# Kernel tuning notes

Hardware: AMD Instinct MI355X
Metric: run time of the kernel (lower is better)

## Reference

```python
import jax, jax.numpy as jnp
import numpy as np

MIN_SIZE = 16.0 / 800.0
PRE_NMS_TOP_K = 6000   # mode='test'
POST_NMS_TOP_K = 300   # mode='test'
IOU_THR = 0.7
H = W = 100
A = 9
N = H * W * A


def setup_inputs() -> dict:
    key = jax.random.key(0)
    k1, k2, k3 = jax.random.split(key, 3)
    pred_cls = jax.random.normal(k1, (1, H, W, 2 * A), dtype=jnp.float32)
    pred_reg = jax.random.normal(k2, (1, N, 4), dtype=jnp.float32) * 0.2
    # anchors as valid normalized xyxy boxes
    u = jax.random.uniform(k3, (N, 4), dtype=jnp.float32)
    cx = 0.05 + 0.9 * u[:, 0]
    cy = 0.05 + 0.9 * u[:, 1]
    w = 0.02 + 0.18 * u[:, 2]
    h = 0.02 + 0.18 * u[:, 3]
    anchor = jnp.stack([cx - w / 2, cy - h / 2, cx + w / 2, cy + h / 2], axis=1)
    return {"pred_cls": pred_cls, "pred_reg": pred_reg, "anchor": anchor}


def greedy_nms_mask(boxes, valid):
    # boxes: [K,4] sorted by descending score; valid: [K] bool
    K = boxes.shape[0]
    area = (boxes[:, 2] - boxes[:, 0]) * (boxes[:, 3] - boxes[:, 1])
    lt = jnp.maximum(boxes[:, None, :2], boxes[None, :, :2])   # [K,K,2]
    rb = jnp.minimum(boxes[:, None, 2:], boxes[None, :, 2:])
    wh = jnp.clip(rb - lt, 0.0)
    inter = wh[..., 0] * wh[..., 1]
    union = area[:, None] + area[None, :] - inter
    iou = inter / jnp.maximum(union, jnp.float32(1e-12))       # [K,K]
    idx = jnp.arange(K)

    def body(i, suppressed):
        keep_i = jnp.logical_not(suppressed[i]) & valid[i]
        return suppressed | (keep_i & (iou[i] > IOU_THR) & (idx > i))

    suppressed = jax.lax.fori_loop(0, K, body, jnp.zeros((K,), dtype=bool))
    return jnp.logical_not(suppressed) & valid


def reference(pred_cls, pred_reg, anchor):
    reg = pred_reg.reshape(-1, 4)                 # squeeze -> [N,4]
    # xy_to_cxcy(anchor)
    a_cxcy = jnp.concatenate([(anchor[:, 2:] + anchor[:, :2]) / 2,
                              anchor[:, 2:] - anchor[:, :2]], axis=1)
    # decode(reg, anchor_cxcy)
    cxcy = reg[:, :2] * a_cxcy[:, 2:] + a_cxcy[:, :2]
    wh = jnp.exp(reg[:, 2:]) * a_cxcy[:, 2:]
    # cxcy_to_xy(...).clamp(0,1)
    roi = jnp.clip(jnp.concatenate([cxcy - wh / 2, cxcy + wh / 2], axis=1), 0.0, 1.0)

    # objectness softmax over the 2-class logits
    probs = jax.nn.softmax(pred_cls.reshape(1, H, W, A, 2), axis=-1)[..., 1].reshape(-1)  # [N]

    # size filter
    ws = roi[:, 2] - roi[:, 0]
    hs = roi[:, 3] - roi[:, 1]
    size_ok = (hs >= MIN_SIZE) & (ws >= MIN_SIZE)
    masked_scores = jnp.where(size_ok, probs, -jnp.inf)

    # sort descending + take pre-NMS top-k (filtered boxes sort last)
    top_scores, top_idx = jax.lax.top_k(masked_scores, PRE_NMS_TOP_K)
    boxes = roi[top_idx]                           # [K,4]
    valid = size_ok[top_idx]

    kept = greedy_nms_mask(boxes, valid)           # [K] bool

    # first POST_NMS_TOP_K kept boxes in score order; pad with zeros
    rank = jnp.cumsum(kept.astype(jnp.int32)) - 1
    slot = jnp.where(kept & (rank < POST_NMS_TOP_K), rank, POST_NMS_TOP_K)
    out = jnp.zeros((POST_NMS_TOP_K, 4), dtype=boxes.dtype).at[slot].set(boxes, mode='drop')
    return out
```

## Files before the change

### kernel.cpp

```cpp
#include <hip/hip_runtime.h>
#include <stdint.h>

#pragma clang fp contract(off)

#define N_ANCH 90000
#define M_TOP  1024
#define M_L    512
#define NW_L   8
#define K_POST 300
#define CAP    2048
#define WINB   0x3D00
#define WINSZ  768
#define MIN_SIZE (16.0f / 800.0f)
#define IOU_THR  0.7f

#define NB_D 88
#define NB_C 32
#define GPB  704

#define SIDX(j) ((j) + ((j) >> 6))
#define SB_SZ   (M_L + NW_L)

#define OFF_CNT   0
#define OFF_HIST  64
#define OFF_MASK  64
#define OFF_CAND  135232
#define OFF_ROI   151616
#define OFF_KEYS  1591616
#define OFF_SBOX  1591616

__global__ void __launch_bounds__(1024)
decode_kernel(const float2* __restrict__ cls,
              const float4* __restrict__ reg,
              const float4* __restrict__ anc,
              float4* __restrict__ roi,
              unsigned* __restrict__ keys,
              unsigned short* __restrict__ hist,
              int* __restrict__ cnt) {
    __shared__ int lh[WINSZ];
    const int tid = threadIdx.x;
    const int bid = blockIdx.x;
    if (tid < WINSZ) lh[tid] = 0;
    if (bid == 0 && tid == 0) cnt[0] = 0;
    __syncthreads();

    const int n = bid * 1024 + tid;
    if (n < N_ANCH) {
        float4 a = anc[n];
        float4 r = reg[n];
        float aw  = a.z - a.x;
        float ah  = a.w - a.y;
        float acx = (a.z + a.x) * 0.5f;
        float acy = (a.w + a.y) * 0.5f;
        float cx = r.x * aw + acx;
        float cy = r.y * ah + acy;
        float w  = expf(r.z) * aw;
        float h  = expf(r.w) * ah;
        float x1 = fminf(fmaxf(cx - w * 0.5f, 0.0f), 1.0f);
        float y1 = fminf(fmaxf(cy - h * 0.5f, 0.0f), 1.0f);
        float x2 = fminf(fmaxf(cx + w * 0.5f, 0.0f), 1.0f);
        float y2 = fminf(fmaxf(cy + h * 0.5f, 0.0f), 1.0f);
        roi[n] = make_float4(x1, y1, x2, y2);

        float2 c = cls[n];
        float m  = fmaxf(c.x, c.y);
        float e0 = expf(c.x - m);
        float e1 = expf(c.y - m);
        float p  = e1 / (e0 + e1);

        bool ok = ((x2 - x1) >= MIN_SIZE) && ((y2 - y1) >= MIN_SIZE);
        unsigned key = ok ? (__float_as_uint(p) ^ 0x80000000u) : 0u;
        keys[n] = key;
        if (key != 0u) {
            int hb = (int)(key >> 16) - 0x8000;
            if (hb >= WINB) atomicAdd(&lh[hb - WINB], 1);
        }
    }
    __syncthreads();
    if (tid < WINSZ) hist[tid * NB_D + bid] = (unsigned short)lh[tid];
}

__global__ void __launch_bounds__(1024)
compact_kernel(const unsigned* __restrict__ keys,
               const unsigned short* __restrict__ hist,
               int* __restrict__ cnt,
               unsigned long long* __restrict__ cand) {
    __shared__ int rscan[1024];
    __shared__ unsigned s_thr;
    __shared__ int wcnt[16], wbase[16];
    __shared__ int s_base;
    const int t = threadIdx.x;

    int wsum = 0;
    if (t < WINSZ) {
        const int bin = WINSZ - 1 - t;
        const uint4* hp = (const uint4*)(hist + bin * NB_D);
#pragma unroll
        for (int q = 0; q < 11; ++q) {
            uint4 v = hp[q];
            wsum += (int)((v.x & 0xffffu) + (v.x >> 16) + (v.y & 0xffffu) + (v.y >> 16)
                        + (v.z & 0xffffu) + (v.z >> 16) + (v.w & 0xffffu) + (v.w >> 16));
        }
    }
    rscan[t] = wsum;
    __syncthreads();
    for (int off = 1; off < 1024; off <<= 1) {
        int add = (t >= off) ? rscan[t - off] : 0;
        __syncthreads();
        rscan[t] += add;
        __syncthreads();
    }
    if (t < WINSZ && rscan[t] >= M_TOP && (t == 0 || rscan[t - 1] < M_TOP))
        s_thr = ((unsigned)(0x8000 + WINB + (WINSZ - 1 - t))) << 16;
    if (t == 0 && rscan[WINSZ - 1] < M_TOP)
        s_thr = 0x80000000u;
    __syncthreads();
    const unsigned thr = s_thr;

    const uint4* k4 = (const uint4*)keys;
    const int g = blockIdx.x * GPB + t;
    const int gend0 = (blockIdx.x + 1) * GPB;
    const int gend = (gend0 < N_ANCH / 4) ? gend0 : (N_ANCH / 4);
    unsigned pm = 0;
    uint4 kv = make_uint4(0u, 0u, 0u, 0u);
    if (t < GPB && g < gend) {
        kv = k4[g];
        pm = (kv.x >= thr ? 1u : 0u) | (kv.y >= thr ? 2u : 0u)
           | (kv.z >= thr ? 4u : 0u) | (kv.w >= thr ? 8u : 0u);
    }
    unsigned long long b0 = __ballot((pm & 1u) != 0u);
    unsigned long long b1 = __ballot((pm & 2u) != 0u);
    unsigned long long b2 = __ballot((pm & 4u) != 0u);
    unsigned long long b3 = __ballot((pm & 8u) != 0u);
    const int ln = t & 63, wv = t >> 6;
    if (ln == 0)
        wcnt[wv] = __popcll(b0) + __popcll(b1) + __popcll(b2) + __popcll(b3);
    __syncthreads();
    if (t == 0) {
        int s = 0;
#pragma unroll
        for (int q = 0; q < 16; ++q) { wbase[q] = s; s += wcnt[q]; }
        s_base = s ? atomicAdd(cnt, s) : 0;
    }
    __syncthreads();
    if (pm) {
        unsigned long long lt = (ln == 0) ? 0ull : ((1ull << ln) - 1ull);
        int pos = s_base + wbase[wv]
                + __popcll(b0 & lt) + __popcll(b1 & lt) + __popcll(b2 & lt) + __popcll(b3 & lt);
        int n0 = g * 4;
        if (pm & 1u) { if (pos < CAP) cand[pos] = ((unsigned long long)kv.x << 32) | (unsigned)(~(unsigned)n0);       ++pos; }
        if (pm & 2u) { if (pos < CAP) cand[pos] = ((unsigned long long)kv.y << 32) | (unsigned)(~(unsigned)(n0 + 1)); ++pos; }
        if (pm & 4u) { if (pos < CAP) cand[pos] = ((unsigned long long)kv.z << 32) | (unsigned)(~(unsigned)(n0 + 2)); ++pos; }
        if (pm & 8u) { if (pos < CAP) cand[pos] = ((unsigned long long)kv.w << 32) | (unsigned)(~(unsigned)(n0 + 3)); ++pos; }
    }
}

__global__ void __launch_bounds__(1024)
rank_select_kernel(const unsigned long long* __restrict__ cand,
                   const int* __restrict__ cnt,
                   const float4* __restrict__ roi,
                   float4* __restrict__ sbox) {
    __shared__ unsigned long long s[CAP];
    __shared__ int red[1024];
    int tid = threadIdx.x;
    int c = cnt[0];
    if (c > CAP) c = CAP;
    for (int k = tid; k < CAP; k += 1024) s[k] = (k < c) ? cand[k] : 0ULL;
    __syncthreads();
    int e = tid & 63;
    int slice = tid >> 6;
    int i = blockIdx.x * 64 + e;
    unsigned long long v = (i < c) ? s[i] : 0ULL;
    int cnt_gt = 0;
    if (i < c) {
        int kbeg = slice * (CAP / 16);
        int kend = kbeg + (CAP / 16);
        if (kend > c) kend = c;
#pragma unroll 4
        for (int k = kbeg; k < kend; ++k)
            cnt_gt += (s[k] > v) ? 1 : 0;
    }
    red[tid] = cnt_gt;
    __syncthreads();
    if (slice == 0 && i < c) {
        int rank = 0;
#pragma unroll
        for (int q = 0; q < 16; ++q) rank += red[e + 64 * q];
        if (rank < M_TOP) {
            unsigned idx = ~((unsigned)v);
            sbox[rank] = roi[idx];
        }
    }
}

__global__ void __launch_bounds__(256)
mask_kernel(const float4* __restrict__ sbox,
            unsigned long long* __restrict__ mask) {
    __shared__ float4 sb[SB_SZ];
    int tid = threadIdx.x;
#pragma unroll
    for (int q = 0; q < M_L / 256; ++q) {
        int j = tid + q * 256;
        sb[SIDX(j)] = sbox[j];
    }
    __syncthreads();
    int wid = blockIdx.x * 256 + tid;
    int i = wid >> 3;
    int w = wid & 7;
    unsigned long long bits = 0;
    int j0 = w << 6;
    if (j0 + 63 > i) {
        float4 bi = sb[SIDX(i)];
        float ai = (bi.z - bi.x) * (bi.w - bi.y);
        for (int b = 0; b < 64; ++b) {
            int j = j0 + b;
            if (j > i) {
                float4 bj = sb[SIDX(j)];
                float xx1 = fmaxf(bi.x, bj.x);
                float yy1 = fmaxf(bi.y, bj.y);
                float xx2 = fminf(bi.z, bj.z);
                float yy2 = fminf(bi.w, bj.w);
                float ww = fmaxf(xx2 - xx1, 0.0f);
                float hh = fmaxf(yy2 - yy1, 0.0f);
                float inter = ww * hh;
                float aj = (bj.z - bj.x) * (bj.w - bj.y);
                float uni = ai + aj - inter;
                float iou = inter / fmaxf(uni, 1e-12f);
                if (iou > IOU_THR) bits |= 1ull << b;
            }
        }
    }
    mask[wid] = bits;
}

__device__ __forceinline__ unsigned long long readlane64(unsigned long long v, int sl) {
    unsigned lo = (unsigned)__builtin_amdgcn_readlane((int)(unsigned)v, sl);
    unsigned hi = (unsigned)__builtin_amdgcn_readlane((int)(unsigned)(v >> 32), sl);
    return ((unsigned long long)hi << 32) | lo;
}

__global__ void __launch_bounds__(256)
walk_kernel(const unsigned long long* __restrict__ mask,
            const float4* __restrict__ sbox,
            const int* __restrict__ cnt,
            float4* __restrict__ out) {
    __shared__ unsigned long long lmask[M_L * NW_L];
    __shared__ int s_keep[K_POST];
    __shared__ int s_kc;
    const int tid = threadIdx.x;

    {
        const uint4* src = (const uint4*)mask;
        uint4* dst = (uint4*)lmask;
#pragma unroll
        for (int q = 0; q < (M_L * NW_L) / 2 / 256; ++q)
            dst[tid + q * 256] = src[tid + q * 256];
    }
    __syncthreads();

    if (tid < 64) {
        int lane = tid;
        int c_eff = cnt[0];
        if (c_eff > M_TOP) c_eff = M_TOP;

        unsigned long long diag[NW_L];
#pragma unroll
        for (int cc = 0; cc < NW_L; ++cc)
            diag[cc] = lmask[(((cc << 6) | lane) << 3) + cc];

        unsigned long long remw = 0;
        int w = lane & 7;
        int kgrp = lane >> 3;
        int kc = 0;
        bool stop = false;
#pragma unroll
        for (int cc = 0; cc < NW_L; ++cc) {
            int base = cc << 6;
            unsigned long long valid =
                (c_eff >= base + 64) ? ~0ull
              : ((c_eff <= base) ? 0ull : ((1ull << (c_eff - base)) - 1ull));
            unsigned long long live = valid & ~readlane64(remw, cc);
            unsigned long long keptbits = 0;
            while (live) {
                int b = __ffsll((unsigned long long)live) - 1;
                keptbits |= 1ull << b;
                if (lane == 0) s_keep[kc] = base + b;
                ++kc;
                if (kc >= K_POST) { stop = true; break; }
                live &= ~readlane64(diag[cc], b);
                live &= ~(1ull << b);
            }
            if (stop) break;
            if (cc == NW_L - 1) break;
            if (keptbits) {
                int nk = __popcll(keptbits);
                int mypos = 0;
                if (lane < nk) {
                    unsigned long long tmp = keptbits;
                    for (int p = 0; p < lane; ++p) tmp &= tmp - 1;
                    mypos = base + (__ffsll((unsigned long long)tmp) - 1);
                }
                unsigned long long acc = 0;
#pragma unroll
                for (int r = 0; r < 8; ++r) {
                    int kg = (r << 3) | kgrp;
                    int row = __shfl(mypos, kg);
                    unsigned long long v = (kg < nk) ? lmask[(row << 3) + w] : 0ull;
                    acc |= v;
                }
                acc |= __shfl_xor(acc, 8);
                acc |= __shfl_xor(acc, 16);
                acc |= __shfl_xor(acc, 32);
                remw |= acc;
            }
        }
        if (!stop) {
            for (int i = M_L; i < c_eff && kc < K_POST; ++i) {
                float4 bi = sbox[i];
                float ai = (bi.z - bi.x) * (bi.w - bi.y);
                bool any = false;
                for (int k = lane; k < kc; k += 64) {
                    float4 bk = sbox[s_keep[k]];
                    float xx1 = fmaxf(bi.x, bk.x);
                    float yy1 = fmaxf(bi.y, bk.y);
                    float xx2 = fminf(bi.z, bk.z);
                    float yy2 = fminf(bi.w, bk.w);
                    float ww = fmaxf(xx2 - xx1, 0.0f);
                    float hh = fmaxf(yy2 - yy1, 0.0f);
                    float inter = ww * hh;
                    float ak = (bk.z - bk.x) * (bk.w - bk.y);
                    float uni = ai + ak - inter;
                    if (inter / fmaxf(uni, 1e-12f) > IOU_THR) any = true;
                }
                if (__ballot(any) == 0ull) {
                    if (lane == 0) s_keep[kc] = i;
                    ++kc;
                }
            }
        }
        if (lane == 0) s_kc = kc;
    }
    __syncthreads();
    int kcf = s_kc;
    for (int j = tid; j < K_POST; j += 256)
        out[j] = (j < kcf) ? sbox[s_keep[j]] : make_float4(0.f, 0.f, 0.f, 0.f);
}

extern "C" void kernel_launch(void* const* d_in, const int* in_sizes, int n_in,
                              void* d_out, int out_size, void* d_ws, size_t ws_size,
                              hipStream_t stream) {
    const float2* cls = (const float2*)d_in[0];
    const float4* reg = (const float4*)d_in[1];
    const float4* anc = (const float4*)d_in[2];
    float4* out = (float4*)d_out;

    char* ws = (char*)d_ws;
    int*                cnt  = (int*)(ws + OFF_CNT);
    unsigned short*     hist = (unsigned short*)(ws + OFF_HIST);
    unsigned long long* mask = (unsigned long long*)(ws + OFF_MASK);
    unsigned long long* cand = (unsigned long long*)(ws + OFF_CAND);
    float4*             roi  = (float4*)(ws + OFF_ROI);
    unsigned*           keys = (unsigned*)(ws + OFF_KEYS);
    float4*             sbox = (float4*)(ws + OFF_SBOX);

    decode_kernel<<<NB_D, 1024, 0, stream>>>(cls, reg, anc, roi, keys, hist, cnt);
    compact_kernel<<<NB_C, 1024, 0, stream>>>(keys, hist, cnt, cand);
    rank_select_kernel<<<CAP / 64, 1024, 0, stream>>>(cand, cnt, roi, sbox);
    mask_kernel<<<M_L * NW_L / 256, 256, 0, stream>>>(sbox, mask);
    walk_kernel<<<1, 256, 0, stream>>>(mask, sbox, cnt, out);
}
```

Before: 123.1 us.

## Fuse compaction, bitonic sort and IoU mask into one redundant-per-block kernel

Merges the compact, rank-select and mask kernels into a single kernel. Each of 16 blocks redundantly scans all keys, does a deterministic prefix-sum compaction into shared memory, bitonic-sorts 2048 candidates, gathers the top boxes and computes its slice of the IoU mask. The decode kernel now runs as 176 blocks of 512 threads. This removes two kernel launches, the global atomic counter and the candidate round trip through global memory. In exchange every block rereads all keys twice and repeats the sort, so the redundant work can cost more than the launches it saves.

```diff
diff --git a/kernel.cpp b/kernel.cpp
--- a/kernel.cpp
+++ b/kernel.cpp
@@ -14,37 +14,34 @@
 #define MIN_SIZE (16.0f / 800.0f)
 #define IOU_THR  0.7f
 
-#define NB_D 88
-#define NB_C 32
-#define GPB  704
+#define NB_D   176
+#define NB_S   16
+#define G4     (N_ANCH / 4)
 
 #define SIDX(j) ((j) + ((j) >> 6))
 #define SB_SZ   (M_L + NW_L)
 
 #define OFF_CNT   0
 #define OFF_HIST  64
-#define OFF_MASK  64
-#define OFF_CAND  135232
-#define OFF_ROI   151616
-#define OFF_KEYS  1591616
-#define OFF_SBOX  1591616
-
-__global__ void __launch_bounds__(1024)
+#define OFF_ROI   270400
+#define OFF_KEYS  1710400
+#define OFF_MASK  2070400
+#define OFF_SBOX  2103168
+
+__global__ void __launch_bounds__(512)
 decode_kernel(const float2* __restrict__ cls,
               const float4* __restrict__ reg,
               const float4* __restrict__ anc,
               float4* __restrict__ roi,
               unsigned* __restrict__ keys,
-              unsigned short* __restrict__ hist,
-              int* __restrict__ cnt) {
+              unsigned short* __restrict__ hist) {
     __shared__ int lh[WINSZ];
     const int tid = threadIdx.x;
     const int bid = blockIdx.x;
-    if (tid < WINSZ) lh[tid] = 0;
-    if (bid == 0 && tid == 0) cnt[0] = 0;
-    __syncthreads();
-
-    const int n = bid * 1024 + tid;
+    for (int k = tid; k < WINSZ; k += 512) lh[k] = 0;
+    __syncthreads();
+
+    const int n = bid * 512 + tid;
     if (n < N_ANCH) {
         float4 a = anc[n];
         float4 r = reg[n];
@@ -77,26 +74,30 @@
         }
     }
     __syncthreads();
-    if (tid < WINSZ) hist[tid * NB_D + bid] = (unsigned short)lh[tid];
+    for (int k = tid; k < WINSZ; k += 512)
+        hist[k * NB_D + bid] = (unsigned short)lh[k];
 }
 
 __global__ void __launch_bounds__(1024)
-compact_kernel(const unsigned* __restrict__ keys,
-               const unsigned short* __restrict__ hist,
-               int* __restrict__ cnt,
-               unsigned long long* __restrict__ cand) {
+sortmask_kernel(const unsigned* __restrict__ keys,
+                const unsigned short* __restrict__ hist,
+                const float4* __restrict__ roi,
+                float4* __restrict__ sbox,
+                int* __restrict__ cnt,
+                unsigned long long* __restrict__ mask) {
     __shared__ int rscan[1024];
     __shared__ unsigned s_thr;
-    __shared__ int wcnt[16], wbase[16];
-    __shared__ int s_base;
+    __shared__ unsigned long long sc[CAP];
+    __shared__ float4 sb[SB_SZ];
     const int t = threadIdx.x;
+    const int bid = blockIdx.x;
 
     int wsum = 0;
     if (t < WINSZ) {
         const int bin = WINSZ - 1 - t;
         const uint4* hp = (const uint4*)(hist + bin * NB_D);
 #pragma unroll
-        for (int q = 0; q < 11; ++q) {
+        for (int q = 0; q < NB_D / 8; ++q) {
             uint4 v = hp[q];
             wsum += (int)((v.x & 0xffffu) + (v.x >> 16) + (v.y & 0xffffu) + (v.y >> 16)
                         + (v.z & 0xffffu) + (v.z >> 16) + (v.w & 0xffffu) + (v.w >> 16));
@@ -118,119 +119,95 @@
     const unsigned thr = s_thr;
 
     const uint4* k4 = (const uint4*)keys;
-    const int g = blockIdx.x * GPB + t;
-    const int gend0 = (blockIdx.x + 1) * GPB;
-    const int gend = (gend0 < N_ANCH / 4) ? gend0 : (N_ANCH / 4);
-    unsigned pm = 0;
-    uint4 kv = make_uint4(0u, 0u, 0u, 0u);
-    if (t < GPB && g < gend) {
-        kv = k4[g];
-        pm = (kv.x >= thr ? 1u : 0u) | (kv.y >= thr ? 2u : 0u)
-           | (kv.z >= thr ? 4u : 0u) | (kv.w >= thr ? 8u : 0u);
-    }
-    unsigned long long b0 = __ballot((pm & 1u) != 0u);
-    unsigned long long b1 = __ballot((pm & 2u) != 0u);
-    unsigned long long b2 = __ballot((pm & 4u) != 0u);
-    unsigned long long b3 = __ballot((pm & 8u) != 0u);
-    const int ln = t & 63, wv = t >> 6;
-    if (ln == 0)
-        wcnt[wv] = __popcll(b0) + __popcll(b1) + __popcll(b2) + __popcll(b3);
-    __syncthreads();
-    if (t == 0) {
-        int s = 0;
-#pragma unroll
-        for (int q = 0; q < 16; ++q) { wbase[q] = s; s += wcnt[q]; }
-        s_base = s ? atomicAdd(cnt, s) : 0;
-    }
-    __syncthreads();
-    if (pm) {
-        unsigned long long lt = (ln == 0) ? 0ull : ((1ull << ln) - 1ull);
-        int pos = s_base + wbase[wv]
-                + __popcll(b0 & lt) + __popcll(b1 & lt) + __popcll(b2 & lt) + __popcll(b3 & lt);
-        int n0 = g * 4;
-        if (pm & 1u) { if (pos < CAP) cand[pos] = ((unsigned long long)kv.x << 32) | (unsigned)(~(unsigned)n0);       ++pos; }
-        if (pm & 2u) { if (pos < CAP) cand[pos] = ((unsigned long long)kv.y << 32) | (unsigned)(~(unsigned)(n0 + 1)); ++pos; }
-        if (pm & 4u) { if (pos < CAP) cand[pos] = ((unsigned long long)kv.z << 32) | (unsigned)(~(unsigned)(n0 + 2)); ++pos; }
-        if (pm & 8u) { if (pos < CAP) cand[pos] = ((unsigned long long)kv.w << 32) | (unsigned)(~(unsigned)(n0 + 3)); ++pos; }
-    }
-}
-
-__global__ void __launch_bounds__(1024)
-rank_select_kernel(const unsigned long long* __restrict__ cand,
-                   const int* __restrict__ cnt,
-                   const float4* __restrict__ roi,
-                   float4* __restrict__ sbox) {
-    __shared__ unsigned long long s[CAP];
-    __shared__ int red[1024];
-    int tid = threadIdx.x;
-    int c = cnt[0];
-    if (c > CAP) c = CAP;
-    for (int k = tid; k < CAP; k += 1024) s[k] = (k < c) ? cand[k] : 0ULL;
-    __syncthreads();
-    int e = tid & 63;
-    int slice = tid >> 6;
-    int i = blockIdx.x * 64 + e;
-    unsigned long long v = (i < c) ? s[i] : 0ULL;
-    int cnt_gt = 0;
-    if (i < c) {
-        int kbeg = slice * (CAP / 16);
-        int kend = kbeg + (CAP / 16);
-        if (kend > c) kend = c;
-#pragma unroll 4
-        for (int k = kbeg; k < kend; ++k)
-            cnt_gt += (s[k] > v) ? 1 : 0;
-    }
-    red[tid] = cnt_gt;
-    __syncthreads();
-    if (slice == 0 && i < c) {
-        int rank = 0;
-#pragma unroll
-        for (int q = 0; q < 16; ++q) rank += red[e + 64 * q];
-        if (rank < M_TOP) {
-            unsigned idx = ~((unsigned)v);
-            sbox[rank] = roi[idx];
-        }
-    }
-}
-
-__global__ void __launch_bounds__(256)
-mask_kernel(const float4* __restrict__ sbox,
-            unsigned long long* __restrict__ mask) {
-    __shared__ float4 sb[SB_SZ];
-    int tid = threadIdx.x;
-#pragma unroll
-    for (int q = 0; q < M_L / 256; ++q) {
-        int j = tid + q * 256;
-        sb[SIDX(j)] = sbox[j];
-    }
-    __syncthreads();
-    int wid = blockIdx.x * 256 + tid;
-    int i = wid >> 3;
-    int w = wid & 7;
-    unsigned long long bits = 0;
-    int j0 = w << 6;
-    if (j0 + 63 > i) {
-        float4 bi = sb[SIDX(i)];
-        float ai = (bi.z - bi.x) * (bi.w - bi.y);
-        for (int b = 0; b < 64; ++b) {
-            int j = j0 + b;
-            if (j > i) {
-                float4 bj = sb[SIDX(j)];
-                float xx1 = fmaxf(bi.x, bj.x);
-                float yy1 = fmaxf(bi.y, bj.y);
-                float xx2 = fminf(bi.z, bj.z);
-                float yy2 = fminf(bi.w, bj.w);
-                float ww = fmaxf(xx2 - xx1, 0.0f);
-                float hh = fmaxf(yy2 - yy1, 0.0f);
-                float inter = ww * hh;
-                float aj = (bj.z - bj.x) * (bj.w - bj.y);
-                float uni = ai + aj - inter;
-                float iou = inter / fmaxf(uni, 1e-12f);
-                if (iou > IOU_THR) bits |= 1ull << b;
+    int mycnt = 0;
+#pragma unroll
+    for (int q = 0; q < 22; ++q) {
+        int g = q * 1024 + t;
+        if (g < G4) {
+            uint4 kv = k4[g];
+            mycnt += (kv.x >= thr) + (kv.y >= thr) + (kv.z >= thr) + (kv.w >= thr);
+        }
+    }
+    __syncthreads();
+    rscan[t] = mycnt;
+    __syncthreads();
+    for (int off = 1; off < 1024; off <<= 1) {
+        int add = (t >= off) ? rscan[t - off] : 0;
+        __syncthreads();
+        rscan[t] += add;
+        __syncthreads();
+    }
+    int base = rscan[t] - mycnt;
+    const int ctot = rscan[1023];
+    const int c = (ctot < CAP) ? ctot : CAP;
+#pragma unroll
+    for (int q = 0; q < 22; ++q) {
+        int g = q * 1024 + t;
+        if (g < G4) {
+            uint4 kv = k4[g];
+            int n0 = g * 4;
+            if (kv.x >= thr) { if (base < CAP) sc[base] = ((unsigned long long)kv.x << 32) | (unsigned)(~(unsigned)n0);       ++base; }
+            if (kv.y >= thr) { if (base < CAP) sc[base] = ((unsigned long long)kv.y << 32) | (unsigned)(~(unsigned)(n0 + 1)); ++base; }
+            if (kv.z >= thr) { if (base < CAP) sc[base] = ((unsigned long long)kv.z << 32) | (unsigned)(~(unsigned)(n0 + 2)); ++base; }
+            if (kv.w >= thr) { if (base < CAP) sc[base] = ((unsigned long long)kv.w << 32) | (unsigned)(~(unsigned)(n0 + 3)); ++base; }
+        }
+    }
+    for (int k = t; k < CAP; k += 1024)
+        if (k >= c) sc[k] = 0ULL;
+    __syncthreads();
+
+    for (int kk = 2; kk <= CAP; kk <<= 1) {
+        for (int j = kk >> 1; j > 0; j >>= 1) {
+            int e = ((t & ~(j - 1)) << 1) | (t & (j - 1));
+            int p = e | j;
+            unsigned long long a = sc[e], b = sc[p];
+            bool desc = ((e & kk) == 0);
+            if (desc ? (a < b) : (a > b)) { sc[e] = b; sc[p] = a; }
+            __syncthreads();
+        }
+    }
+
+    if (t < M_L) {
+        unsigned long long v = sc[t];
+        float4 bx = (t < c) ? roi[~(unsigned)v] : make_float4(0.f, 0.f, 0.f, 0.f);
+        sb[SIDX(t)] = bx;
+        if (bid == 0) sbox[t] = bx;
+    } else if (bid == 0) {
+        unsigned long long v = sc[t];
+        sbox[t] = (t < c) ? roi[~(unsigned)v] : make_float4(0.f, 0.f, 0.f, 0.f);
+    }
+    if (bid == 0 && t == 0) cnt[0] = c;
+    __syncthreads();
+
+    if (t < 256) {
+        int wid = bid * 256 + t;
+        int i = wid >> 3;
+        int w = wid & 7;
+        unsigned long long bits = 0;
+        int j0 = w << 6;
+        if (j0 + 63 > i) {
+            float4 bi = sb[SIDX(i)];
+            float ai = (bi.z - bi.x) * (bi.w - bi.y);
+            for (int b = 0; b < 64; ++b) {
+                int j = j0 + b;
+                if (j > i) {
+                    float4 bj = sb[SIDX(j)];
+                    float xx1 = fmaxf(bi.x, bj.x);
+                    float yy1 = fmaxf(bi.y, bj.y);
+                    float xx2 = fminf(bi.z, bj.z);
+                    float yy2 = fminf(bi.w, bj.w);
+                    float ww = fmaxf(xx2 - xx1, 0.0f);
+                    float hh = fmaxf(yy2 - yy1, 0.0f);
+                    float inter = ww * hh;
+                    float aj = (bj.z - bj.x) * (bj.w - bj.y);
+                    float uni = ai + aj - inter;
+                    float iou = inter / fmaxf(uni, 1e-12f);
+                    if (iou > IOU_THR) bits |= 1ull << b;
+                }
             }
         }
-    }
-    mask[wid] = bits;
+        mask[wid] = bits;
+    }
 }
 
 __device__ __forceinline__ unsigned long long readlane64(unsigned long long v, int sl) {
@@ -357,15 +334,12 @@
     char* ws = (char*)d_ws;
     int*                cnt  = (int*)(ws + OFF_CNT);
     unsigned short*     hist = (unsigned short*)(ws + OFF_HIST);
-    unsigned long long* mask = (unsigned long long*)(ws + OFF_MASK);
-    unsigned long long* cand = (unsigned long long*)(ws + OFF_CAND);
     float4*             roi  = (float4*)(ws + OFF_ROI);
     unsigned*           keys = (unsigned*)(ws + OFF_KEYS);
+    unsigned long long* mask = (unsigned long long*)(ws + OFF_MASK);
     float4*             sbox = (float4*)(ws + OFF_SBOX);
 
-    decode_kernel<<<NB_D, 1024, 0, stream>>>(cls, reg, anc, roi, keys, hist, cnt);
-    compact_kernel<<<NB_C, 1024, 0, stream>>>(keys, hist, cnt, cand);
-    rank_select_kernel<<<CAP / 64, 1024, 0, stream>>>(cand, cnt, roi, sbox);
-    mask_kernel<<<M_L * NW_L / 256, 256, 0, stream>>>(sbox, mask);
+    decode_kernel<<<NB_D, 512, 0, stream>>>(cls, reg, anc, roi, keys, hist);
+    sortmask_kernel<<<NB_S, 1024, 0, stream>>>(keys, hist, roi, sbox, cnt, mask);
     walk_kernel<<<1, 256, 0, stream>>>(mask, sbox, cnt, out);
 }
```

Result: slower. 144.6 us (+17.4%).

## Fuse compact, rank-select, mask and walk into one kernel with grid barriers

Applied to the files above, without the earlier changes.

Merges four launches (compaction, rank selection, IoU mask build and greedy walk) into a single 32-block kernel. A spin-wait atomic counter serves as a grid barrier between compaction and ranking, and a last-block-done counter hands the mask build and walk to the final block. The histogram prefix scan now uses wave shuffles instead of a shared-memory Hillis-Steele loop, and decode runs as 176 blocks of 512 threads. The aim is to remove launch gaps between small kernels. The cost is that the mask is built by one block instead of 16, and the spin barrier relies on all 32 blocks being co-resident.

```diff
diff --git a/kernel.cpp b/kernel.cpp
--- a/kernel.cpp
+++ b/kernel.cpp
@@ -14,37 +14,41 @@
 #define MIN_SIZE (16.0f / 800.0f)
 #define IOU_THR  0.7f
 
-#define NB_D 88
-#define NB_C 32
-#define GPB  704
+#define NB_D   176
+#define NB_S   32
+#define GPB    704
+#define G4     (N_ANCH / 4)
 
 #define SIDX(j) ((j) + ((j) >> 6))
 #define SB_SZ   (M_L + NW_L)
 
 #define OFF_CNT   0
-#define OFF_HIST  64
-#define OFF_MASK  64
-#define OFF_CAND  135232
-#define OFF_ROI   151616
-#define OFF_KEYS  1591616
-#define OFF_SBOX  1591616
-
-__global__ void __launch_bounds__(1024)
+#define OFF_D1    64
+#define OFF_D2    128
+#define OFF_HIST  192
+#define OFF_ROI   270528
+#define OFF_KEYS  1710528
+#define OFF_CAND  2070528
+#define OFF_SBOX  2086912
+
+__global__ void __launch_bounds__(512)
 decode_kernel(const float2* __restrict__ cls,
               const float4* __restrict__ reg,
               const float4* __restrict__ anc,
               float4* __restrict__ roi,
               unsigned* __restrict__ keys,
               unsigned short* __restrict__ hist,
-              int* __restrict__ cnt) {
+              int* __restrict__ cnt,
+              int* __restrict__ d1,
+              int* __restrict__ d2) {
     __shared__ int lh[WINSZ];
     const int tid = threadIdx.x;
     const int bid = blockIdx.x;
-    if (tid < WINSZ) lh[tid] = 0;
-    if (bid == 0 && tid == 0) cnt[0] = 0;
-    __syncthreads();
-
-    const int n = bid * 1024 + tid;
+    for (int k = tid; k < WINSZ; k += 512) lh[k] = 0;
+    if (bid == 0 && tid == 0) { cnt[0] = 0; d1[0] = 0; d2[0] = 0; }
+    __syncthreads();
+
+    const int n = bid * 512 + tid;
     if (n < N_ANCH) {
         float4 a = anc[n];
         float4 r = reg[n];
@@ -77,54 +81,67 @@
         }
     }
     __syncthreads();
-    if (tid < WINSZ) hist[tid * NB_D + bid] = (unsigned short)lh[tid];
+    for (int k = tid; k < WINSZ; k += 512)
+        hist[k * NB_D + bid] = (unsigned short)lh[k];
 }
 
+__device__ __forceinline__ unsigned long long readlane64(unsigned long long v, int sl) {
+    unsigned lo = (unsigned)__builtin_amdgcn_readlane((int)(unsigned)v, sl);
+    unsigned hi = (unsigned)__builtin_amdgcn_readlane((int)(unsigned)(v >> 32), sl);
+    return ((unsigned long long)hi << 32) | lo;
+}
+
 __global__ void __launch_bounds__(1024)
-compact_kernel(const unsigned* __restrict__ keys,
-               const unsigned short* __restrict__ hist,
-               int* __restrict__ cnt,
-               unsigned long long* __restrict__ cand) {
-    __shared__ int rscan[1024];
+select_kernel(const unsigned* __restrict__ keys,
+              const unsigned short* __restrict__ hist,
+              const float4* __restrict__ roi,
+              int* cnt,
+              unsigned long long* cand,
+              float4* sbox,
+              int* d1,
+              int* d2,
+              float4* __restrict__ out) {
+    __shared__ __align__(16) char arena[8320 + 32768];
+    __shared__ int s_w[16];
     __shared__ unsigned s_thr;
-    __shared__ int wcnt[16], wbase[16];
-    __shared__ int s_base;
+    __shared__ int wcnt[16], wbase[16], s_base;
+    __shared__ int s_last;
+    __shared__ int s_keep[K_POST];
+    __shared__ int s_kc;
     const int t = threadIdx.x;
-
-    int wsum = 0;
+    const int bid = blockIdx.x;
+    const int lane = t & 63, wv = t >> 6;
+
+    int own = 0;
     if (t < WINSZ) {
-        const int bin = WINSZ - 1 - t;
-        const uint4* hp = (const uint4*)(hist + bin * NB_D);
-#pragma unroll
-        for (int q = 0; q < 11; ++q) {
-            uint4 v = hp[q];
-            wsum += (int)((v.x & 0xffffu) + (v.x >> 16) + (v.y & 0xffffu) + (v.y >> 16)
-                        + (v.z & 0xffffu) + (v.z >> 16) + (v.w & 0xffffu) + (v.w >> 16));
-        }
-    }
-    rscan[t] = wsum;
-    __syncthreads();
-    for (int off = 1; off < 1024; off <<= 1) {
-        int add = (t >= off) ? rscan[t - off] : 0;
-        __syncthreads();
-        rscan[t] += add;
-        __syncthreads();
-    }
-    if (t < WINSZ && rscan[t] >= M_TOP && (t == 0 || rscan[t - 1] < M_TOP))
+        const uint4* hp = (const uint4*)(hist + (WINSZ - 1 - t) * NB_D);
+#pragma unroll
+        for (int q = 0; q < NB_D / 8; ++q) {
+            uint4 u = hp[q];
+            own += (int)((u.x & 0xffffu) + (u.x >> 16) + (u.y & 0xffffu) + (u.y >> 16)
+                       + (u.z & 0xffffu) + (u.z >> 16) + (u.w & 0xffffu) + (u.w >> 16));
+        }
+    }
+    int x = own;
+#pragma unroll
+    for (int d = 1; d < 64; d <<= 1) { int y = __shfl_up(x, d); if (lane >= d) x += y; }
+    if (lane == 63) s_w[wv] = x;
+    __syncthreads();
+    int incl = x;
+#pragma unroll
+    for (int q = 0; q < 16; ++q) if (q < wv) incl += s_w[q];
+    if (t < WINSZ && incl >= M_TOP && (incl - own) < M_TOP)
         s_thr = ((unsigned)(0x8000 + WINB + (WINSZ - 1 - t))) << 16;
-    if (t == 0 && rscan[WINSZ - 1] < M_TOP)
+    if (t == 1023 && incl < M_TOP)
         s_thr = 0x80000000u;
     __syncthreads();
     const unsigned thr = s_thr;
 
-    const uint4* k4 = (const uint4*)keys;
-    const int g = blockIdx.x * GPB + t;
-    const int gend0 = (blockIdx.x + 1) * GPB;
-    const int gend = (gend0 < N_ANCH / 4) ? gend0 : (N_ANCH / 4);
     unsigned pm = 0;
     uint4 kv = make_uint4(0u, 0u, 0u, 0u);
-    if (t < GPB && g < gend) {
-        kv = k4[g];
+    const int g = bid * GPB + t;
+    if (t < GPB && g < G4) {
+        kv = ((const uint4*)keys)[g];
         pm = (kv.x >= thr ? 1u : 0u) | (kv.y >= thr ? 2u : 0u)
            | (kv.z >= thr ? 4u : 0u) | (kv.w >= thr ? 8u : 0u);
     }
@@ -132,8 +149,7 @@
     unsigned long long b1 = __ballot((pm & 2u) != 0u);
     unsigned long long b2 = __ballot((pm & 4u) != 0u);
     unsigned long long b3 = __ballot((pm & 8u) != 0u);
-    const int ln = t & 63, wv = t >> 6;
-    if (ln == 0)
+    if (lane == 0)
         wcnt[wv] = __popcll(b0) + __popcll(b1) + __popcll(b2) + __popcll(b3);
     __syncthreads();
     if (t == 0) {
@@ -144,7 +160,7 @@
     }
     __syncthreads();
     if (pm) {
-        unsigned long long lt = (ln == 0) ? 0ull : ((1ull << ln) - 1ull);
+        unsigned long long lt = (lane == 0) ? 0ull : ((1ull << lane) - 1ull);
         int pos = s_base + wbase[wv]
                 + __popcll(b0 & lt) + __popcll(b1 & lt) + __popcll(b2 & lt) + __popcll(b3 & lt);
         int n0 = g * 4;
@@ -153,124 +169,106 @@
         if (pm & 4u) { if (pos < CAP) cand[pos] = ((unsigned long long)kv.z << 32) | (unsigned)(~(unsigned)(n0 + 2)); ++pos; }
         if (pm & 8u) { if (pos < CAP) cand[pos] = ((unsigned long long)kv.w << 32) | (unsigned)(~(unsigned)(n0 + 3)); ++pos; }
     }
-}
-
-__global__ void __launch_bounds__(1024)
-rank_select_kernel(const unsigned long long* __restrict__ cand,
-                   const int* __restrict__ cnt,
-                   const float4* __restrict__ roi,
-                   float4* __restrict__ sbox) {
-    __shared__ unsigned long long s[CAP];
-    __shared__ int red[1024];
-    int tid = threadIdx.x;
-    int c = cnt[0];
+
+    __syncthreads();
+    __threadfence();
+    if (t == 0) {
+        __hip_atomic_fetch_add(d1, 1, __ATOMIC_ACQ_REL, __HIP_MEMORY_SCOPE_AGENT);
+        while (__hip_atomic_load(d1, __ATOMIC_ACQUIRE, __HIP_MEMORY_SCOPE_AGENT) < NB_S)
+            __builtin_amdgcn_s_sleep(2);
+    }
+    __syncthreads();
+    __threadfence();
+
+    unsigned long long* sc = (unsigned long long*)arena;
+    int* red = (int*)(arena + CAP * 8);
+    int c = __hip_atomic_load(cnt, __ATOMIC_RELAXED, __HIP_MEMORY_SCOPE_AGENT);
     if (c > CAP) c = CAP;
-    for (int k = tid; k < CAP; k += 1024) s[k] = (k < c) ? cand[k] : 0ULL;
-    __syncthreads();
-    int e = tid & 63;
-    int slice = tid >> 6;
-    int i = blockIdx.x * 64 + e;
-    unsigned long long v = (i < c) ? s[i] : 0ULL;
-    int cnt_gt = 0;
-    if (i < c) {
-        int kbeg = slice * (CAP / 16);
-        int kend = kbeg + (CAP / 16);
-        if (kend > c) kend = c;
+    for (int k = t; k < CAP; k += 1024)
+        sc[k] = (k < c) ? __hip_atomic_load(&cand[k], __ATOMIC_RELAXED, __HIP_MEMORY_SCOPE_AGENT)
+                        : 0ULL;
+    __syncthreads();
+    {
+        int e = t & 63, slice = t >> 6;
+        int i = bid * 64 + e;
+        unsigned long long v = (i < c) ? sc[i] : 0ULL;
+        int cg = 0;
+        if (i < c) {
+            int kb = slice * (CAP / 16), ke = kb + CAP / 16;
+            if (ke > c) ke = c;
 #pragma unroll 4
-        for (int k = kbeg; k < kend; ++k)
-            cnt_gt += (s[k] > v) ? 1 : 0;
-    }
-    red[tid] = cnt_gt;
-    __syncthreads();
-    if (slice == 0 && i < c) {
-        int rank = 0;
-#pragma unroll
-        for (int q = 0; q < 16; ++q) rank += red[e + 64 * q];
-        if (rank < M_TOP) {
-            unsigned idx = ~((unsigned)v);
-            sbox[rank] = roi[idx];
-        }
-    }
-}
-
-__global__ void __launch_bounds__(256)
-mask_kernel(const float4* __restrict__ sbox,
-            unsigned long long* __restrict__ mask) {
-    __shared__ float4 sb[SB_SZ];
-    int tid = threadIdx.x;
-#pragma unroll
-    for (int q = 0; q < M_L / 256; ++q) {
-        int j = tid + q * 256;
-        sb[SIDX(j)] = sbox[j];
-    }
-    __syncthreads();
-    int wid = blockIdx.x * 256 + tid;
-    int i = wid >> 3;
-    int w = wid & 7;
-    unsigned long long bits = 0;
-    int j0 = w << 6;
-    if (j0 + 63 > i) {
-        float4 bi = sb[SIDX(i)];
-        float ai = (bi.z - bi.x) * (bi.w - bi.y);
-        for (int b = 0; b < 64; ++b) {
-            int j = j0 + b;
-            if (j > i) {
-                float4 bj = sb[SIDX(j)];
-                float xx1 = fmaxf(bi.x, bj.x);
-                float yy1 = fmaxf(bi.y, bj.y);
-                float xx2 = fminf(bi.z, bj.z);
-                float yy2 = fminf(bi.w, bj.w);
-                float ww = fmaxf(xx2 - xx1, 0.0f);
-                float hh = fmaxf(yy2 - yy1, 0.0f);
-                float inter = ww * hh;
-                float aj = (bj.z - bj.x) * (bj.w - bj.y);
-                float uni = ai + aj - inter;
-                float iou = inter / fmaxf(uni, 1e-12f);
-                if (iou > IOU_THR) bits |= 1ull << b;
+            for (int k = kb; k < ke; ++k) cg += (sc[k] > v) ? 1 : 0;
+        }
+        red[t] = cg;
+        __syncthreads();
+        if (slice == 0 && i < c) {
+            int rank = 0;
+#pragma unroll
+            for (int q = 0; q < 16; ++q) rank += red[e + 64 * q];
+            if (rank < M_TOP) sbox[rank] = roi[~(unsigned)v];
+        }
+    }
+
+    __syncthreads();
+    __threadfence();
+    if (t == 0) {
+        int old = __hip_atomic_fetch_add(d2, 1, __ATOMIC_ACQ_REL, __HIP_MEMORY_SCOPE_AGENT);
+        s_last = (old == NB_S - 1);
+    }
+    __syncthreads();
+    if (!s_last) return;
+    __threadfence();
+
+    float4* sb = (float4*)arena;
+    unsigned long long* lmask = (unsigned long long*)(arena + 8320);
+    if (t < M_L)
+        sb[SIDX(t)] = (t < c) ? sbox[t] : make_float4(0.f, 0.f, 0.f, 0.f);
+    __syncthreads();
+#pragma unroll
+    for (int q = 0; q < 4; ++q) {
+        int wid = q * 1024 + t;
+        int i = wid >> 3;
+        int w = wid & 7;
+        unsigned long long bits = 0;
+        int j0 = w << 6;
+        if (j0 + 63 > i) {
+            float4 bi = sb[SIDX(i)];
+            float ai = (bi.z - bi.x) * (bi.w - bi.y);
+            for (int b = 0; b < 64; ++b) {
+                int j = j0 + b;
+                if (j > i) {
+                    float4 bj = sb[SIDX(j)];
+                    float xx1 = fmaxf(bi.x, bj.x);
+                    float yy1 = fmaxf(bi.y, bj.y);
+                    float xx2 = fminf(bi.z, bj.z);
+                    float yy2 = fminf(bi.w, bj.w);
+                    float ww = fmaxf(xx2 - xx1, 0.0f);
+                    float hh = fmaxf(yy2 - yy1, 0.0f);
+                    float inter = ww * hh;
+                    float aj = (bj.z - bj.x) * (bj.w - bj.y);
+                    float uni = ai + aj - inter;
+                    float iou = inter / fmaxf(uni, 1e-12f);
+                    if (iou > IOU_THR) bits |= 1ull << b;
+                }
             }
         }
-    }
-    mask[wid] = bits;
-}
-
-__device__ __forceinline__ unsigned long long readlane64(unsigned long long v, int sl) {
-    unsigned lo = (unsigned)__builtin_amdgcn_readlane((int)(unsigned)v, sl);
-    unsigned hi = (unsigned)__builtin_amdgcn_readlane((int)(unsigned)(v >> 32), sl);
-    return ((unsigned long long)hi << 32) | lo;
-}
-
-__global__ void __launch_bounds__(256)
-walk_kernel(const unsigned long long* __restrict__ mask,
-            const float4* __restrict__ sbox,
-            const int* __restrict__ cnt,
-            float4* __restrict__ out) {
-    __shared__ unsigned long long lmask[M_L * NW_L];
-    __shared__ int s_keep[K_POST];
-    __shared__ int s_kc;
-    const int tid = threadIdx.x;
-
-    {
-        const uint4* src = (const uint4*)mask;
-        uint4* dst = (uint4*)lmask;
-#pragma unroll
-        for (int q = 0; q < (M_L * NW_L) / 2 / 256; ++q)
-            dst[tid + q * 256] = src[tid + q * 256];
-    }
-    __syncthreads();
-
-    if (tid < 64) {
-        int lane = tid;
-        int c_eff = cnt[0];
+        lmask[wid] = bits;
+    }
+    __syncthreads();
+
+    if (t < 64) {
+        int wl = t;
+        int c_eff = c;
         if (c_eff > M_TOP) c_eff = M_TOP;
 
         unsigned long long diag[NW_L];
 #pragma unroll
         for (int cc = 0; cc < NW_L; ++cc)
-            diag[cc] = lmask[(((cc << 6) | lane) << 3) + cc];
+            diag[cc] = lmask[(((cc << 6) | wl) << 3) + cc];
 
         unsigned long long remw = 0;
-        int w = lane & 7;
-        int kgrp = lane >> 3;
+        int w = wl & 7;
+        int kgrp = wl >> 3;
         int kc = 0;
         bool stop = false;
 #pragma unroll
@@ -284,7 +282,7 @@
             while (live) {
                 int b = __ffsll((unsigned long long)live) - 1;
                 keptbits |= 1ull << b;
-                if (lane == 0) s_keep[kc] = base + b;
+                if (wl == 0) s_keep[kc] = base + b;
                 ++kc;
                 if (kc >= K_POST) { stop = true; break; }
                 live &= ~readlane64(diag[cc], b);
@@ -295,9 +293,9 @@
             if (keptbits) {
                 int nk = __popcll(keptbits);
                 int mypos = 0;
-                if (lane < nk) {
+                if (wl < nk) {
                     unsigned long long tmp = keptbits;
-                    for (int p = 0; p < lane; ++p) tmp &= tmp - 1;
+                    for (int p = 0; p < wl; ++p) tmp &= tmp - 1;
                     mypos = base + (__ffsll((unsigned long long)tmp) - 1);
                 }
                 unsigned long long acc = 0;
@@ -305,8 +303,8 @@
                 for (int r = 0; r < 8; ++r) {
                     int kg = (r << 3) | kgrp;
                     int row = __shfl(mypos, kg);
-                    unsigned long long v = (kg < nk) ? lmask[(row << 3) + w] : 0ull;
-                    acc |= v;
+                    unsigned long long vv = (kg < nk) ? lmask[(row << 3) + w] : 0ull;
+                    acc |= vv;
                 }
                 acc |= __shfl_xor(acc, 8);
                 acc |= __shfl_xor(acc, 16);
@@ -319,7 +317,7 @@
                 float4 bi = sbox[i];
                 float ai = (bi.z - bi.x) * (bi.w - bi.y);
                 bool any = false;
-                for (int k = lane; k < kc; k += 64) {
+                for (int k = wl; k < kc; k += 64) {
                     float4 bk = sbox[s_keep[k]];
                     float xx1 = fmaxf(bi.x, bk.x);
                     float yy1 = fmaxf(bi.y, bk.y);
@@ -333,16 +331,16 @@
                     if (inter / fmaxf(uni, 1e-12f) > IOU_THR) any = true;
                 }
                 if (__ballot(any) == 0ull) {
-                    if (lane == 0) s_keep[kc] = i;
+                    if (wl == 0) s_keep[kc] = i;
                     ++kc;
                 }
             }
         }
-        if (lane == 0) s_kc = kc;
+        if (wl == 0) s_kc = kc;
     }
     __syncthreads();
     int kcf = s_kc;
-    for (int j = tid; j < K_POST; j += 256)
+    for (int j = t; j < K_POST; j += 1024)
         out[j] = (j < kcf) ? sbox[s_keep[j]] : make_float4(0.f, 0.f, 0.f, 0.f);
 }
 
@@ -356,16 +354,14 @@
 
     char* ws = (char*)d_ws;
     int*                cnt  = (int*)(ws + OFF_CNT);
+    int*                d1   = (int*)(ws + OFF_D1);
+    int*                d2   = (int*)(ws + OFF_D2);
     unsigned short*     hist = (unsigned short*)(ws + OFF_HIST);
-    unsigned long long* mask = (unsigned long long*)(ws + OFF_MASK);
-    unsigned long long* cand = (unsigned long long*)(ws + OFF_CAND);
     float4*             roi  = (float4*)(ws + OFF_ROI);
     unsigned*           keys = (unsigned*)(ws + OFF_KEYS);
+    unsigned long long* cand = (unsigned long long*)(ws + OFF_CAND);
     float4*             sbox = (float4*)(ws + OFF_SBOX);
 
-    decode_kernel<<<NB_D, 1024, 0, stream>>>(cls, reg, anc, roi, keys, hist, cnt);
-    compact_kernel<<<NB_C, 1024, 0, stream>>>(keys, hist, cnt, cand);
-    rank_select_kernel<<<CAP / 64, 1024, 0, stream>>>(cand, cnt, roi, sbox);
-    mask_kernel<<<M_L * NW_L / 256, 256, 0, stream>>>(sbox, mask);
-    walk_kernel<<<1, 256, 0, stream>>>(mask, sbox, cnt, out);
+    decode_kernel<<<NB_D, 512, 0, stream>>>(cls, reg, anc, roi, keys, hist, cnt, d1, d2);
+    select_kernel<<<NB_S, 1024, 0, stream>>>(keys, hist, roi, cnt, cand, sbox, d1, d2, out);
 }
```

Result: slower. 191.2 us (+55.3%).
